# Kernel tuning notes

Hardware: AMD Instinct MI355X
Metric: run time of the kernel (lower is better)

## Reference

```python
import jax, jax.numpy as jnp
import numpy as np

B, FIN, FOUT, FH = 32, 32, 32, 64
H = W = 128
LAT = 512
K_IN, K_MID, K_OUT, K_SHORT = FH * FIN, FH * FH, FOUT * FH, FOUT * FIN
K_TOTAL = K_IN + K_MID + K_OUT + K_SHORT + FH + FH + FOUT + FOUT  # 9408


def setup_inputs() -> dict:
    key = jax.random.key(0)
    ks = jax.random.split(key, 20)
    def rn(k, shape, scale=None):
        s = scale if scale is not None else 1.0 / np.sqrt(shape[-1])
        return jax.random.normal(k, shape, dtype=jnp.float32) * s
    return {
        "x": jax.random.normal(ks[0], (B, FIN, H, W), dtype=jnp.float32),
        "lat": jax.random.normal(ks[1], (B, LAT), dtype=jnp.float32),
        "w0": rn(ks[2], (LAT, LAT)), "b0": rn(ks[3], (LAT,), 0.02),
        "w1a": rn(ks[4], (2 * LAT, LAT)), "b1a": rn(ks[5], (2 * LAT,), 0.02),
        "w1b": rn(ks[6], (LAT, 2 * LAT)), "b1b": rn(ks[7], (LAT,), 0.02),
        "w1s": rn(ks[8], (LAT, LAT)), "b1s": rn(ks[9], (LAT,), 0.02),
        "w2a": rn(ks[10], (2 * LAT, LAT)), "b2a": rn(ks[11], (2 * LAT,), 0.02),
        "w2b": rn(ks[12], (K_TOTAL, 2 * LAT)), "b2b": rn(ks[13], (K_TOTAL,), 0.02),
        "w2s": rn(ks[14], (K_TOTAL, LAT)), "b2s": rn(ks[15], (K_TOTAL,), 0.02),
        "wfa": rn(ks[16], (K_TOTAL, K_TOTAL)), "bfa": rn(ks[17], (K_TOTAL,), 0.02),
    }


def _lrb(h, wa, ba, wb, bb, ws, bs):
    # LinearResidualBlock: shortcut + 2-layer MLP with ReLU
    return h @ ws.T + bs + jax.nn.relu(h @ wa.T + ba) @ wb.T + bb


def reference(x, lat, w0, b0, w1a, b1a, w1b, b1b, w1s, b1s,
              w2a, b2a, w2b, b2b, w2s, b2s, wfa, bfa):
    # hypernetwork: dyna_k then LinearFA (forward is a plain linear)
    h = lat @ w0.T + b0                              # [B, 512]
    h = _lrb(h, w1a, b1a, w1b, b1b, w1s, b1s)        # [B, 512]
    h = _lrb(h, w2a, b2a, w2b, b2b, w2s, b2s)        # [B, K_TOTAL]
    ks = h @ wfa.T + bfa                             # [B, K_TOTAL]

    sizes = [K_IN, K_MID, K_OUT, K_SHORT, FH, FH, FOUT, FOUT]
    offs = np.cumsum([0] + sizes)
    k_in = ks[:, offs[0]:offs[1]].reshape(B, FH, FIN)
    k_mid = ks[:, offs[1]:offs[2]].reshape(B, FH, FH)
    k_out = ks[:, offs[2]:offs[3]].reshape(B, FOUT, FH)
    k_short = ks[:, offs[3]:offs[4]].reshape(B, FOUT, FIN)
    b_in = ks[:, offs[4]:offs[5]][:, :, None, None]    # [B, FH, 1, 1]
    b_mid = ks[:, offs[5]:offs[6]][:, :, None, None]
    b_out = ks[:, offs[6]:offs[7]][:, :, None, None]   # [B, FOUT, 1, 1]
    b_short = ks[:, offs[7]:offs[8]][:, :, None, None]

    # per-sample 1x1 grouped convs == batched matmuls over channels
    xs = jnp.einsum('bihw,boi->bohw', x, k_short) + b_short
    xn = jax.nn.relu(jnp.einsum('bihw,boi->bohw', x, k_in) + b_in)
    xn = jax.nn.relu(jnp.einsum('bihw,boi->bohw', xn, k_mid) + b_mid)
    xn = jnp.einsum('bihw,boi->bohw', xn, k_out) + b_out
    return xn + xs
```

## Files before the change

kernel.cpp:

```cpp
#include <hip/hip_runtime.h>
#include <cstdint>

#define KT 9408
#define NT 256
#define KC 16

__global__ __launch_bounds__(256, 1) void gemm32_partial(
    const float* __restrict__ X1, const float* __restrict__ W1, int K1,
    const float* __restrict__ X2, const float* __restrict__ W2, int K2,
    float* __restrict__ partial, int O, int ksplit)
{
    __shared__ float Xs[KC][32];
    __shared__ float Wt[KC][NT];

    const int t      = threadIdx.x;
    const int o0     = blockIdx.x * NT;
    const int s      = blockIdx.y;
    const int kchunk = (K1 + K2) / ksplit;
    const int kbeg   = s * kchunk;
    const int kend   = kbeg + kchunk;
    const int lane   = t & 63;
    const int wv     = t >> 6;

    const int sr  = t >> 2;
    const int sc4 = (t & 3) << 2;

    float4 wpre[4];
    float  xpre[2];

    {
        int kc0 = kbeg;
#pragma unroll
        for (int p = 0; p < 4; ++p) {
            int r = sr + 64 * p;
            int o = o0 + r;
            int kg = kc0 + sc4;
            float4 v = make_float4(0.f, 0.f, 0.f, 0.f);
            if (o < O)
                v = (kg < K1) ? *(const float4*)&W1[(size_t)o * K1 + kg]
                              : *(const float4*)&W2[(size_t)o * K2 + (kg - K1)];
            wpre[p] = v;
        }
#pragma unroll
        for (int it = 0; it < 2; ++it) {
            int idx = t + 256 * it;
            int kg  = kc0 + (idx >> 5);
            int bb  = idx & 31;
            xpre[it] = (kg < K1) ? X1[(size_t)bb * K1 + kg]
                                 : X2[(size_t)bb * K2 + (kg - K1)];
        }
    }

    float acc[8][4];
#pragma unroll
    for (int bi = 0; bi < 8; bi++)
#pragma unroll
        for (int j = 0; j < 4; j++) acc[bi][j] = 0.f;

    for (int kc0 = kbeg; kc0 < kend; kc0 += KC) {
#pragma unroll
        for (int it = 0; it < 2; ++it) {
            int idx = t + 256 * it;
            Xs[idx >> 5][idx & 31] = xpre[it];
        }
#pragma unroll
        for (int p = 0; p < 4; ++p) {
            int r = sr + 64 * p;
            Wt[sc4 + 0][r] = wpre[p].x;
            Wt[sc4 + 1][r] = wpre[p].y;
            Wt[sc4 + 2][r] = wpre[p].z;
            Wt[sc4 + 3][r] = wpre[p].w;
        }
        __syncthreads();

        if (kc0 + KC < kend) {
            int kn = kc0 + KC;
#pragma unroll
            for (int p = 0; p < 4; ++p) {
                int r = sr + 64 * p;
                int o = o0 + r;
                int kg = kn + sc4;
                float4 v = make_float4(0.f, 0.f, 0.f, 0.f);
                if (o < O)
                    v = (kg < K1) ? *(const float4*)&W1[(size_t)o * K1 + kg]
                                  : *(const float4*)&W2[(size_t)o * K2 + (kg - K1)];
                wpre[p] = v;
            }
#pragma unroll
            for (int it = 0; it < 2; ++it) {
                int idx = t + 256 * it;
                int kg  = kn + (idx >> 5);
                int bb  = idx & 31;
                xpre[it] = (kg < K1) ? X1[(size_t)bb * K1 + kg]
                                     : X2[(size_t)bb * K2 + (kg - K1)];
            }
        }

#pragma unroll
        for (int c = 0; c < KC; c++) {
            float4 xa = *(const float4*)&Xs[c][wv * 8];
            float4 xb = *(const float4*)&Xs[c][wv * 8 + 4];
            float xv[8] = {xa.x, xa.y, xa.z, xa.w, xb.x, xb.y, xb.z, xb.w};
            float w[4];
#pragma unroll
            for (int j = 0; j < 4; j++) w[j] = Wt[c][lane + 64 * j];
#pragma unroll
            for (int bi = 0; bi < 8; bi++)
#pragma unroll
                for (int j = 0; j < 4; j++) acc[bi][j] += xv[bi] * w[j];
        }
        __syncthreads();
    }

#pragma unroll
    for (int bi = 0; bi < 8; bi++) {
        int b = wv * 8 + bi;
#pragma unroll
        for (int j = 0; j < 4; j++) {
            int o = o0 + lane + 64 * j;
            if (o < O)
                partial[((size_t)s * 32 + b) * O + o] = acc[bi][j];
        }
    }
}

__global__ __launch_bounds__(256) void reduce_bias(
    const float* __restrict__ partial, const float* __restrict__ bias1,
    const float* __restrict__ bias2, float* __restrict__ Y, int O, int relu,
    int ksplit)
{
    int idx = blockIdx.x * 256 + threadIdx.x;
    if (idx >= 32 * O) return;
    int b = idx / O, o = idx - b * O;
    float s = bias1[o] + (bias2 ? bias2[o] : 0.f);
    for (int k = 0; k < ksplit; k++)
        s += partial[((size_t)k * 32 + b) * O + o];
    Y[idx] = relu ? fmaxf(s, 0.f) : s;
}

typedef __attribute__((ext_vector_type(8))) short bf16x8;
typedef __attribute__((ext_vector_type(4))) float f32x4;

__device__ inline uint32_t pkbf(float lo, float hi) {
    uint32_t a = __builtin_bit_cast(uint32_t, lo);
    uint32_t b = __builtin_bit_cast(uint32_t, hi);
    a = (a + 0x7FFFu + ((a >> 16) & 1u)) >> 16;
    b = (b + 0x7FFFu + ((b >> 16) & 1u)) & 0xFFFF0000u;
    return a | b;
}
__device__ inline uint32_t pk_hi(float a, float b, float& ra, float& rb) {
    uint32_t ua = __builtin_bit_cast(uint32_t, a);
    uint32_t ub = __builtin_bit_cast(uint32_t, b);
    uint32_t ha = (ua + 0x7FFFu + ((ua >> 16) & 1u)) & 0xFFFF0000u;
    uint32_t hb = (ub + 0x7FFFu + ((ub >> 16) & 1u)) & 0xFFFF0000u;
    ra = a - __builtin_bit_cast(float, ha);
    rb = b - __builtin_bit_cast(float, hb);
    return (ha >> 16) | hb;
}

#define MFMA16(a, b, c) __builtin_amdgcn_mfma_f32_16x16x32_bf16(a, b, c, 0, 0, 0)

#define GLOAD(SUF, kcv)                                                        \
    {                                                                          \
        int _kc = (kcv);                                                       \
        const float *_Wr, *_Xb; int _kk, _ld;                                  \
        if (_kc < K1) { _Wr = W1; _Xb = X1; _kk = _kc;      _ld = K1; }        \
        else          { _Wr = W2; _Xb = X2; _kk = _kc - K1; _ld = K2; }        \
        const float* _wp = _Wr + (size_t)(o0 + n) * _ld + _kk + 4 * g;         \
        w0##SUF = *(const float4*)_wp;  w1##SUF = *(const float4*)(_wp + 16);  \
        const float* _xp = _Xb + (size_t)n * _ld + _kk + 4 * g;                \
        x0##SUF = *(const float4*)_xp;  x1##SUF = *(const float4*)(_xp + 16);  \
        const float* _yp = _Xb + (size_t)(16 + n) * _ld + _kk + 4 * g;         \
        y0##SUF = *(const float4*)_yp;  y1##SUF = *(const float4*)(_yp + 16);  \
    }

#define GCONS(SUF)                                                             \
    {                                                                          \
        union { bf16x8 v; uint32_t u4[4]; } wf;                                \
        wf.u4[0] = pkbf(w0##SUF.x, w0##SUF.y);                                 \
        wf.u4[1] = pkbf(w0##SUF.z, w0##SUF.w);                                 \
        wf.u4[2] = pkbf(w1##SUF.x, w1##SUF.y);                                 \
        wf.u4[3] = pkbf(w1##SUF.z, w1##SUF.w);                                 \
        float r0, r1, r2, r3, r4, r5, r6, r7;                                  \
        union { bf16x8 v; uint32_t u4[4]; } xh, xl;                            \
        xh.u4[0] = pk_hi(x0##SUF.x, x0##SUF.y, r0, r1);                        \
        xh.u4[1] = pk_hi(x0##SUF.z, x0##SUF.w, r2, r3);                        \
        xh.u4[2] = pk_hi(x1##SUF.x, x1##SUF.y, r4, r5);                        \
        xh.u4[3] = pk_hi(x1##SUF.z, x1##SUF.w, r6, r7);                        \
        xl.u4[0] = pkbf(r0, r1); xl.u4[1] = pkbf(r2, r3);                      \
        xl.u4[2] = pkbf(r4, r5); xl.u4[3] = pkbf(r6, r7);                      \
        accA = MFMA16(xh.v, wf.v, accA);                                       \
        accA = MFMA16(xl.v, wf.v, accA);                                       \
        xh.u4[0] = pk_hi(y0##SUF.x, y0##SUF.y, r0, r1);                        \
        xh.u4[1] = pk_hi(y0##SUF.z, y0##SUF.w, r2, r3);                        \
        xh.u4[2] = pk_hi(y1##SUF.x, y1##SUF.y, r4, r5);                        \
        xh.u4[3] = pk_hi(y1##SUF.z, y1##SUF.w, r6, r7);                        \
        xl.u4[0] = pkbf(r0, r1); xl.u4[1] = pkbf(r2, r3);                      \
        xl.u4[2] = pkbf(r4, r5); xl.u4[3] = pkbf(r6, r7);                      \
        accB = MFMA16(xh.v, wf.v, accB);                                       \
        accB = MFMA16(xl.v, wf.v, accB);                                       \
    }

__global__ __launch_bounds__(256) void gemm32_mfma(
    const float* __restrict__ X1, const float* __restrict__ W1, int K1,
    const float* __restrict__ X2, const float* __restrict__ W2, int K2,
    float* __restrict__ partial, int O, int ksplit)
{
    const int t  = threadIdx.x;
    const int l  = t & 63;
    const int g  = l >> 4;
    const int n  = l & 15;
    const int o0 = blockIdx.x * 64 + (t >> 6) * 16;
    const int s  = blockIdx.y;
    const int kchunk = (K1 + K2) / ksplit;
    const int kbeg   = s * kchunk;
    const int kend   = kbeg + kchunk;

    f32x4 accA, accB;
#pragma unroll
    for (int r = 0; r < 4; ++r) { accA[r] = 0.f; accB[r] = 0.f; }

    float4 w0A, w1A, x0A, x1A, y0A, y1A;
    float4 w0B, w1B, x0B, x1B, y0B, y1B;

    GLOAD(A, kbeg);
    for (int kc = kbeg; kc < kend; kc += 64) {
        GLOAD(B, kc + 32);
        GCONS(A);
        if (kc + 64 < kend) GLOAD(A, kc + 64);
        GCONS(B);
    }

#pragma unroll
    for (int r = 0; r < 4; ++r) {
        partial[((size_t)s * 32 + (4 * g + r)) * O + o0 + n]      = accA[r];
        partial[((size_t)s * 32 + (16 + 4 * g + r)) * O + o0 + n] = accB[r];
    }
}

#define TPW 16

__global__ __launch_bounds__(256, 3) void conv_mfma(
    const float* __restrict__ x, const float* __restrict__ ks,
    float* __restrict__ out)
{
    const int t  = threadIdx.x;
    const int b  = blockIdx.y;
    const int l  = t & 63;
    const int g  = l >> 4;
    const int n  = l & 15;
    const int wid = blockIdx.x * 4 + (t >> 6);

    const float* __restrict__ kb = ks + (size_t)b * KT;
    const float* __restrict__ xbase = x + (size_t)b * 524288 + (size_t)(4 * g) * 16384 + n;
    float* __restrict__ obase = out + (size_t)b * 524288 + (size_t)(4 * g) * 16384 + n;

    float e[8];
    auto loadx = [&](int px0) {
        const float* p = xbase + px0;
        e[0] = p[0]; e[1] = p[16384]; e[2] = p[2 * 16384]; e[3] = p[3 * 16384];
        const float* q = p + (size_t)16 * 16384;
        e[4] = q[0]; e[5] = q[16384]; e[6] = q[2 * 16384]; e[7] = q[3 * 16384];
    };
    loadx(wid * TPW * 16);

    auto loadA = [&](const float* W, int ldw, int row0, int k0) -> bf16x8 {
        const float* p = W + (size_t)(row0 + n) * ldw + k0 + 4 * g;
        float4 lo = *(const float4*)p;
        float4 hi = *(const float4*)(p + 16);
        union { bf16x8 v; uint32_t u[4]; } r;
        r.u[0] = pkbf(lo.x, lo.y);
        r.u[1] = pkbf(lo.z, lo.w);
        r.u[2] = pkbf(hi.x, hi.y);
        r.u[3] = pkbf(hi.z, hi.w);
        return r.v;
    };
    auto loadBias = [&](int off) -> f32x4 {
        float4 v = *(const float4*)&kb[off + 4 * g];
        f32x4 r; r[0] = v.x; r[1] = v.y; r[2] = v.z; r[3] = v.w;
        return r;
    };

    bf16x8 ain[4], amid[4][2], aout[2][2], ashort[2];
#pragma unroll
    for (int rt = 0; rt < 4; ++rt) ain[rt] = loadA(kb, 32, 16 * rt, 0);
#pragma unroll
    for (int ot = 0; ot < 4; ++ot)
#pragma unroll
        for (int kf = 0; kf < 2; ++kf) amid[ot][kf] = loadA(kb + 2048, 64, 16 * ot, 32 * kf);
#pragma unroll
    for (int ot = 0; ot < 2; ++ot)
#pragma unroll
        for (int kf = 0; kf < 2; ++kf) aout[ot][kf] = loadA(kb + 6144, 64, 16 * ot, 32 * kf);
#pragma unroll
    for (int ot = 0; ot < 2; ++ot) ashort[ot] = loadA(kb + 8192, 32, 16 * ot, 0);

    f32x4 bin[4], bmid[4], bos[2];
#pragma unroll
    for (int rt = 0; rt < 4; ++rt) bin[rt] = loadBias(9216 + 16 * rt);
#pragma unroll
    for (int ot = 0; ot < 4; ++ot) bmid[ot] = loadBias(9280 + 16 * ot);
#pragma unroll
    for (int ot = 0; ot < 2; ++ot) {
        f32x4 a = loadBias(9344 + 16 * ot);
        f32x4 c = loadBias(9376 + 16 * ot);
#pragma unroll
        for (int r = 0; r < 4; ++r) a[r] += c[r];
        bos[ot] = a;
    }

#pragma unroll 1
    for (int it = 0; it < TPW; ++it) {
        const int px0 = (wid * TPW + it) * 16;

        union { bf16x8 v; uint32_t u[4]; } bx;
        bx.u[0] = pkbf(e[0], e[1]); bx.u[1] = pkbf(e[2], e[3]);
        bx.u[2] = pkbf(e[4], e[5]); bx.u[3] = pkbf(e[6], e[7]);

        if (it + 1 < TPW) loadx(px0 + 16);

        f32x4 h[4];
#pragma unroll
        for (int rt = 0; rt < 4; ++rt) {
            f32x4 acc = MFMA16(ain[rt], bx.v, bin[rt]);
#pragma unroll
            for (int r = 0; r < 4; ++r) acc[r] = fmaxf(acc[r], 0.f);
            h[rt] = acc;
        }
        union { bf16x8 v; uint32_t u[4]; } hb0, hb1;
        hb0.u[0] = pkbf(h[0][0], h[0][1]); hb0.u[1] = pkbf(h[0][2], h[0][3]);
        hb0.u[2] = pkbf(h[1][0], h[1][1]); hb0.u[3] = pkbf(h[1][2], h[1][3]);
        hb1.u[0] = pkbf(h[2][0], h[2][1]); hb1.u[1] = pkbf(h[2][2], h[2][3]);
        hb1.u[2] = pkbf(h[3][0], h[3][1]); hb1.u[3] = pkbf(h[3][2], h[3][3]);

        f32x4 m[4];
#pragma unroll
        for (int ot = 0; ot < 4; ++ot) {
            f32x4 acc = MFMA16(amid[ot][0], hb0.v, bmid[ot]);
            acc = MFMA16(amid[ot][1], hb1.v, acc);
#pragma unroll
            for (int r = 0; r < 4; ++r) acc[r] = fmaxf(acc[r], 0.f);
            m[ot] = acc;
        }
        union { bf16x8 v; uint32_t u[4]; } mb0, mb1;
        mb0.u[0] = pkbf(m[0][0], m[0][1]); mb0.u[1] = pkbf(m[0][2], m[0][3]);
        mb0.u[2] = pkbf(m[1][0], m[1][1]); mb0.u[3] = pkbf(m[1][2], m[1][3]);
        mb1.u[0] = pkbf(m[2][0], m[2][1]); mb1.u[1] = pkbf(m[2][2], m[2][3]);
        mb1.u[2] = pkbf(m[3][0], m[3][1]); mb1.u[3] = pkbf(m[3][2], m[3][3]);

#pragma unroll
        for (int ot = 0; ot < 2; ++ot) {
            f32x4 acc = MFMA16(ashort[ot], bx.v, bos[ot]);
            acc = MFMA16(aout[ot][0], mb0.v, acc);
            acc = MFMA16(aout[ot][1], mb1.v, acc);
            float* po = obase + (size_t)(16 * ot) * 16384 + px0;
            po[0]         = acc[0];
            po[16384]     = acc[1];
            po[2 * 16384] = acc[2];
            po[3 * 16384] = acc[3];
        }
    }
}

extern "C" void kernel_launch(void* const* d_in, const int* in_sizes, int n_in,
                              void* d_out, int out_size, void* d_ws, size_t ws_size,
                              hipStream_t stream)
{
    const float* x   = (const float*)d_in[0];
    const float* lat = (const float*)d_in[1];
    const float* w0  = (const float*)d_in[2];
    const float* b0  = (const float*)d_in[3];
    const float* w1a = (const float*)d_in[4];
    const float* b1a = (const float*)d_in[5];
    const float* w1b = (const float*)d_in[6];
    const float* b1b = (const float*)d_in[7];
    const float* w1s = (const float*)d_in[8];
    const float* b1s = (const float*)d_in[9];
    const float* w2a = (const float*)d_in[10];
    const float* b2a = (const float*)d_in[11];
    const float* w2b = (const float*)d_in[12];
    const float* b2b = (const float*)d_in[13];
    const float* w2s = (const float*)d_in[14];
    const float* b2s = (const float*)d_in[15];
    const float* wfa = (const float*)d_in[16];
    const float* bfa = (const float*)d_in[17];

    float* ws  = (float*)d_ws;
    float* h0  = ws;
    float* t1  = ws + 16384;
    float* h1  = ws + 49152;
    float* t2  = ws + 65536;
    float* h2  = ws + 98304;
    float* ksb = ws + 399360;
    float* pbuf = (float*)d_out;

    dim3 blk(256);
    auto rg = [](int O) { return dim3((unsigned)((32 * O + 255) / 256)); };

    gemm32_partial<<<dim3(2, 32), blk, 0, stream>>>(lat, w0, 512, nullptr, nullptr, 0, pbuf, 512, 32);
    reduce_bias<<<rg(512), blk, 0, stream>>>(pbuf, b0, nullptr, h0, 512, 0, 32);
    gemm32_partial<<<dim3(4, 32), blk, 0, stream>>>(h0, w1a, 512, nullptr, nullptr, 0, pbuf, 1024, 32);
    reduce_bias<<<rg(1024), blk, 0, stream>>>(pbuf, b1a, nullptr, t1, 1024, 1, 32);
    gemm32_partial<<<dim3(2, 32), blk, 0, stream>>>(h0, w1s, 512, t1, w1b, 1024, pbuf, 512, 32);
    reduce_bias<<<rg(512), blk, 0, stream>>>(pbuf, b1s, b1b, h1, 512, 0, 32);
    gemm32_partial<<<dim3(4, 32), blk, 0, stream>>>(h1, w2a, 512, nullptr, nullptr, 0, pbuf, 1024, 32);
    reduce_bias<<<rg(1024), blk, 0, stream>>>(pbuf, b2a, nullptr, t2, 1024, 1, 32);

    gemm32_mfma<<<dim3(147, 6), blk, 0, stream>>>(h1, w2s, 512, t2, w2b, 1024, pbuf, KT, 6);
    reduce_bias<<<rg(KT), blk, 0, stream>>>(pbuf, b2s, b2b, h2, KT, 0, 6);
    gemm32_mfma<<<dim3(147, 7), blk, 0, stream>>>(h2, wfa, KT, nullptr, nullptr, 0, pbuf, KT, 7);
    reduce_bias<<<rg(KT), blk, 0, stream>>>(pbuf, bfa, nullptr, ksb, KT, 0, 7);

    conv_mfma<<<dim3(16, 32), blk, 0, stream>>>(x, ksb, (float*)d_out);
}
```

Measured before the change: 295.2 us.

## Fuse small hypernetwork layers into one persistent kernel with grid barriers

Replaces the four split-K GEMM launches and four reduce launches for the small MLP layers with a single persistent kernel of 256 blocks. Blocks synchronise through an atomic-counter grid barrier, and each output element is computed by four threads doing float4 dot products followed by a shared-memory reduction. This removes seven kernel launches and the partial-buffer round trips. In exchange it relies on all 256 blocks being co-resident for the spin barrier, adds a memset, and uses a simpler, less reuse-heavy dot-product scheme.

```diff
diff --git a/kernel.cpp b/kernel.cpp
--- a/kernel.cpp
+++ b/kernel.cpp
@@ -2,141 +2,7 @@
 #include <cstdint>
 
 #define KT 9408
-#define NT 256
-#define KC 16
-
-__global__ __launch_bounds__(256, 1) void gemm32_partial(
-    const float* __restrict__ X1, const float* __restrict__ W1, int K1,
-    const float* __restrict__ X2, const float* __restrict__ W2, int K2,
-    float* __restrict__ partial, int O, int ksplit)
-{
-    __shared__ float Xs[KC][32];
-    __shared__ float Wt[KC][NT];
-
-    const int t      = threadIdx.x;
-    const int o0     = blockIdx.x * NT;
-    const int s      = blockIdx.y;
-    const int kchunk = (K1 + K2) / ksplit;
-    const int kbeg   = s * kchunk;
-    const int kend   = kbeg + kchunk;
-    const int lane   = t & 63;
-    const int wv     = t >> 6;
-
-    const int sr  = t >> 2;
-    const int sc4 = (t & 3) << 2;
-
-    float4 wpre[4];
-    float  xpre[2];
-
-    {
-        int kc0 = kbeg;
-#pragma unroll
-        for (int p = 0; p < 4; ++p) {
-            int r = sr + 64 * p;
-            int o = o0 + r;
-            int kg = kc0 + sc4;
-            float4 v = make_float4(0.f, 0.f, 0.f, 0.f);
-            if (o < O)
-                v = (kg < K1) ? *(const float4*)&W1[(size_t)o * K1 + kg]
-                              : *(const float4*)&W2[(size_t)o * K2 + (kg - K1)];
-            wpre[p] = v;
-        }
-#pragma unroll
-        for (int it = 0; it < 2; ++it) {
-            int idx = t + 256 * it;
-            int kg  = kc0 + (idx >> 5);
-            int bb  = idx & 31;
-            xpre[it] = (kg < K1) ? X1[(size_t)bb * K1 + kg]
-                                 : X2[(size_t)bb * K2 + (kg - K1)];
-        }
-    }
-
-    float acc[8][4];
-#pragma unroll
-    for (int bi = 0; bi < 8; bi++)
-#pragma unroll
-        for (int j = 0; j < 4; j++) acc[bi][j] = 0.f;
-
-    for (int kc0 = kbeg; kc0 < kend; kc0 += KC) {
-#pragma unroll
-        for (int it = 0; it < 2; ++it) {
-            int idx = t + 256 * it;
-            Xs[idx >> 5][idx & 31] = xpre[it];
-        }
-#pragma unroll
-        for (int p = 0; p < 4; ++p) {
-            int r = sr + 64 * p;
-            Wt[sc4 + 0][r] = wpre[p].x;
-            Wt[sc4 + 1][r] = wpre[p].y;
-            Wt[sc4 + 2][r] = wpre[p].z;
-            Wt[sc4 + 3][r] = wpre[p].w;
-        }
-        __syncthreads();
-
-        if (kc0 + KC < kend) {
-            int kn = kc0 + KC;
-#pragma unroll
-            for (int p = 0; p < 4; ++p) {
-                int r = sr + 64 * p;
-                int o = o0 + r;
-                int kg = kn + sc4;
-                float4 v = make_float4(0.f, 0.f, 0.f, 0.f);
-                if (o < O)
-                    v = (kg < K1) ? *(const float4*)&W1[(size_t)o * K1 + kg]
-                                  : *(const float4*)&W2[(size_t)o * K2 + (kg - K1)];
-                wpre[p] = v;
-            }
-#pragma unroll
-            for (int it = 0; it < 2; ++it) {
-                int idx = t + 256 * it;
-                int kg  = kn + (idx >> 5);
-                int bb  = idx & 31;
-                xpre[it] = (kg < K1) ? X1[(size_t)bb * K1 + kg]
-                                     : X2[(size_t)bb * K2 + (kg - K1)];
-            }
-        }
-
-#pragma unroll
-        for (int c = 0; c < KC; c++) {
-            float4 xa = *(const float4*)&Xs[c][wv * 8];
-            float4 xb = *(const float4*)&Xs[c][wv * 8 + 4];
-            float xv[8] = {xa.x, xa.y, xa.z, xa.w, xb.x, xb.y, xb.z, xb.w};
-            float w[4];
-#pragma unroll
-            for (int j = 0; j < 4; j++) w[j] = Wt[c][lane + 64 * j];
-#pragma unroll
-            for (int bi = 0; bi < 8; bi++)
-#pragma unroll
-                for (int j = 0; j < 4; j++) acc[bi][j] += xv[bi] * w[j];
-        }
-        __syncthreads();
-    }
-
-#pragma unroll
-    for (int bi = 0; bi < 8; bi++) {
-        int b = wv * 8 + bi;
-#pragma unroll
-        for (int j = 0; j < 4; j++) {
-            int o = o0 + lane + 64 * j;
-            if (o < O)
-                partial[((size_t)s * 32 + b) * O + o] = acc[bi][j];
-        }
-    }
-}
-
-__global__ __launch_bounds__(256) void reduce_bias(
-    const float* __restrict__ partial, const float* __restrict__ bias1,
-    const float* __restrict__ bias2, float* __restrict__ Y, int O, int relu,
-    int ksplit)
-{
-    int idx = blockIdx.x * 256 + threadIdx.x;
-    if (idx >= 32 * O) return;
-    int b = idx / O, o = idx - b * O;
-    float s = bias1[o] + (bias2 ? bias2[o] : 0.f);
-    for (int k = 0; k < ksplit; k++)
-        s += partial[((size_t)k * 32 + b) * O + o];
-    Y[idx] = relu ? fmaxf(s, 0.f) : s;
-}
+#define SNB 256
 
 typedef __attribute__((ext_vector_type(8))) short bf16x8;
 typedef __attribute__((ext_vector_type(4))) float f32x4;
@@ -159,6 +25,90 @@
 }
 
 #define MFMA16(a, b, c) __builtin_amdgcn_mfma_f32_16x16x32_bf16(a, b, c, 0, 0, 0)
+
+__device__ inline void gbar(int* cnt, int target) {
+    __syncthreads();
+    if (threadIdx.x == 0) {
+        __threadfence();
+        __hip_atomic_fetch_add(cnt, 1, __ATOMIC_ACQ_REL, __HIP_MEMORY_SCOPE_AGENT);
+        while (__hip_atomic_load(cnt, __ATOMIC_ACQUIRE, __HIP_MEMORY_SCOPE_AGENT) < target)
+            __builtin_amdgcn_s_sleep(8);
+        __threadfence();
+    }
+    __syncthreads();
+}
+
+__device__ void sstage(const float* __restrict__ X1, const float* __restrict__ W1, int K1,
+                       const float* __restrict__ X2, const float* __restrict__ W2, int K2,
+                       const float* __restrict__ b1v, const float* __restrict__ b2v,
+                       float* __restrict__ Y, int O, bool relu,
+                       int blk, int t, float* red)
+{
+    const int K = K1 + K2;
+    const int iters = K >> 4;
+    const int slots = 32 * O * 4;
+    const int j = t & 3;
+
+    for (int base = blk * 256; base < slots; base += SNB * 256) {
+        int c = (base + t) >> 2;
+        int o = c >> 5, b = c & 31;
+        float acc = 0.f;
+        for (int it = 0; it < iters; ++it) {
+            int kg = it * 16 + j * 4;
+            const float *xp, *wp;
+            if (kg < K1) { xp = X1 + (size_t)b * K1 + kg;        wp = W1 + (size_t)o * K1 + kg; }
+            else         { xp = X2 + (size_t)b * K2 + (kg - K1); wp = W2 + (size_t)o * K2 + (kg - K1); }
+            float4 xv = *(const float4*)xp;
+            float4 wv = *(const float4*)wp;
+            acc += xv.x * wv.x + xv.y * wv.y + xv.z * wv.z + xv.w * wv.w;
+        }
+        red[t] = acc;
+        __syncthreads();
+        if (j == 0) {
+            int rb = t;
+            float s = red[rb] + red[rb + 1] + red[rb + 2] + red[rb + 3];
+            s += b1v[o] + (b2v ? b2v[o] : 0.f);
+            Y[(size_t)b * O + o] = relu ? fmaxf(s, 0.f) : s;
+        }
+        __syncthreads();
+    }
+}
+
+__global__ __launch_bounds__(256, 2) void hyper_small(
+    const float* __restrict__ lat,
+    const float* __restrict__ w0,  const float* __restrict__ b0,
+    const float* __restrict__ w1a, const float* __restrict__ b1a,
+    const float* __restrict__ w1b, const float* __restrict__ b1b,
+    const float* __restrict__ w1s, const float* __restrict__ b1s,
+    const float* __restrict__ w2a, const float* __restrict__ b2a,
+    float* __restrict__ h0, float* __restrict__ t1, float* __restrict__ h1,
+    float* __restrict__ t2, int* __restrict__ cnt)
+{
+    __shared__ float red[256];
+    const int blk = blockIdx.x, t = threadIdx.x;
+
+    sstage(lat, w0, 512, nullptr, nullptr, 0, b0, nullptr, h0, 512, false, blk, t, red);
+    gbar(cnt, 1 * SNB);
+    sstage(h0, w1a, 512, nullptr, nullptr, 0, b1a, nullptr, t1, 1024, true, blk, t, red);
+    gbar(cnt, 2 * SNB);
+    sstage(h0, w1s, 512, t1, w1b, 1024, b1s, b1b, h1, 512, false, blk, t, red);
+    gbar(cnt, 3 * SNB);
+    sstage(h1, w2a, 512, nullptr, nullptr, 0, b2a, nullptr, t2, 1024, true, blk, t, red);
+}
+
+__global__ __launch_bounds__(256) void reduce_bias(
+    const float* __restrict__ partial, const float* __restrict__ bias1,
+    const float* __restrict__ bias2, float* __restrict__ Y, int O, int relu,
+    int ksplit)
+{
+    int idx = blockIdx.x * 256 + threadIdx.x;
+    if (idx >= 32 * O) return;
+    int b = idx / O, o = idx - b * O;
+    float s = bias1[o] + (bias2 ? bias2[o] : 0.f);
+    for (int k = 0; k < ksplit; k++)
+        s += partial[((size_t)k * 32 + b) * O + o];
+    Y[idx] = relu ? fmaxf(s, 0.f) : s;
+}
 
 #define GLOAD(SUF, kcv)                                                        \
     {                                                                          \
@@ -392,19 +342,17 @@
     float* t2  = ws + 65536;
     float* h2  = ws + 98304;
     float* ksb = ws + 399360;
+    int*   cnt = (int*)((char*)d_ws + 4u * 1024u * 1024u);
     float* pbuf = (float*)d_out;
 
     dim3 blk(256);
     auto rg = [](int O) { return dim3((unsigned)((32 * O + 255) / 256)); };
 
-    gemm32_partial<<<dim3(2, 32), blk, 0, stream>>>(lat, w0, 512, nullptr, nullptr, 0, pbuf, 512, 32);
-    reduce_bias<<<rg(512), blk, 0, stream>>>(pbuf, b0, nullptr, h0, 512, 0, 32);
-    gemm32_partial<<<dim3(4, 32), blk, 0, stream>>>(h0, w1a, 512, nullptr, nullptr, 0, pbuf, 1024, 32);
-    reduce_bias<<<rg(1024), blk, 0, stream>>>(pbuf, b1a, nullptr, t1, 1024, 1, 32);
-    gemm32_partial<<<dim3(2, 32), blk, 0, stream>>>(h0, w1s, 512, t1, w1b, 1024, pbuf, 512, 32);
-    reduce_bias<<<rg(512), blk, 0, stream>>>(pbuf, b1s, b1b, h1, 512, 0, 32);
-    gemm32_partial<<<dim3(4, 32), blk, 0, stream>>>(h1, w2a, 512, nullptr, nullptr, 0, pbuf, 1024, 32);
-    reduce_bias<<<rg(1024), blk, 0, stream>>>(pbuf, b2a, nullptr, t2, 1024, 1, 32);
+    hipMemsetAsync(cnt, 0, 4, stream);
+
+    hyper_small<<<dim3(SNB), blk, 0, stream>>>(
+        lat, w0, b0, w1a, b1a, w1b, b1b, w1s, b1s, w2a, b2a,
+        h0, t1, h1, t2, cnt);
 
     gemm32_mfma<<<dim3(147, 6), blk, 0, stream>>>(h1, w2s, 512, t2, w2b, 1024, pbuf, KT, 6);
     reduce_bias<<<rg(KT), blk, 0, stream>>>(pbuf, b2s, b2b, h2, KT, 0, 6);
```

After: 366.6 us. +24.2%, slower.
